# Optimization experiments

Hardware: AMD Instinct MI355X
Metric: run time of the kernel (lower is better)

## Reference

```python
import jax, jax.numpy as jnp
import numpy as np

N_NODES = 50000
N_EDGES = 800000
NFEAT = 512
NHID = 64
NHEADS = 8
NCLASS = 40
ALPHA = 0.2  # LeakyReLU slope
EPS = 1e-16  # guards isolated-node division


def setup_inputs() -> dict:
    key = jax.random.key(0)
    k = jax.random.split(key, 6)
    x = jax.random.normal(k[0], (N_NODES, NFEAT), dtype=jnp.float32)
    W_heads = jax.random.normal(k[1], (NHEADS, NFEAT, NHID), dtype=jnp.float32) * 0.05
    a_heads = jax.random.normal(k[2], (NHEADS, 2 * NHID), dtype=jnp.float32) * 0.05
    W_out = jax.random.normal(k[3], (NHEADS * NHID, NCLASS), dtype=jnp.float32) * 0.05
    a_out = jax.random.normal(k[4], (2 * NCLASS,), dtype=jnp.float32) * 0.05
    edge_index = jax.random.randint(k[5], (2, N_EDGES), 0, N_NODES, dtype=jnp.int32)
    return {"x": x, "W_heads": W_heads, "a_heads": a_heads,
            "W_out": W_out, "a_out": a_out, "edge_index": edge_index}


def _gat_layer(x, W, a, row, col, concat):
    # pyGAT sparse layer: h = xW; e_ij = exp(-LeakyReLU(a^T [h_i || h_j]));
    # out_i = sum_j e_ij h_j / sum_j e_ij   (aggregate into row, gather from col)
    D = W.shape[1]
    h = x @ W                                            # [N, D]
    score = h[row] @ a[:D] + h[col] @ a[D:]              # [E]
    e = jnp.exp(-jax.nn.leaky_relu(score, ALPHA))        # [E]
    num = jax.ops.segment_sum(e[:, None] * h[col], row, num_segments=x.shape[0])  # [N, D]
    den = jax.ops.segment_sum(e, row, num_segments=x.shape[0])                    # [N]
    out = num / (den[:, None] + EPS)
    return jax.nn.elu(out) if concat else out


def reference(x, W_heads, a_heads, W_out, a_out, edge_index):
    # dropout layers are identity in eval mode (training=False)
    row, col = edge_index[0], edge_index[1]
    heads = jax.vmap(lambda W, a: _gat_layer(x, W, a, row, col, True))(W_heads, a_heads)
    # [H, N, D] -> [N, H*D] (concat along feature dim, head-major like torch.cat)
    hcat = jnp.transpose(heads, (1, 0, 2)).reshape(x.shape[0], -1)
    return _gat_layer(hcat, W_out, a_out, row, col, False)  # [N, NCLASS]
```

## Files before the change

### kernel.cpp

```cpp
#include <hip/hip_runtime.h>
#include <hip/hip_bf16.h>

#define N_NODES 50000
#define N_EDGES 800000
#define NFEAT   512
#define NHID    64
#define NHEADS  8
#define NCLASS  40
#define HD      (NHEADS*NHID)
#define ALPHA   0.2f
#define EPS_F   1e-16f
#define NCHUNK  ((N_NODES + 255)/256)

typedef __attribute__((ext_vector_type(8))) short short8;
typedef __attribute__((ext_vector_type(4))) float floatx4;

__device__ __forceinline__ float bf2f(unsigned short u) {
    union { unsigned int i; float f; } v; v.i = ((unsigned int)u) << 16; return v.f;
}
__device__ __forceinline__ unsigned short f2bf(float f) {
    union { __hip_bfloat16 h; unsigned short u; } cv;
    cv.h = __float2bfloat16(f);
    return cv.u;
}

__device__ __forceinline__ void gload16(const unsigned short* g, short* l) {
    __builtin_amdgcn_global_load_lds(
        (const __attribute__((address_space(1))) void*)g,
        (__attribute__((address_space(3))) void*)l,
        16, 0, 0);
}

__global__ __launch_bounds__(256) void prep(const float* __restrict__ x,
                                            unsigned short* __restrict__ xb,
                                            const float* __restrict__ Wh,
                                            unsigned short* __restrict__ Wrb,
                                            const float* __restrict__ Wo,
                                            unsigned short* __restrict__ Wob,
                                            int* __restrict__ deg) {
    int idx = blockIdx.x*256 + threadIdx.x;
    if (idx < N_NODES*64) {
        const float* s = x + (size_t)idx*8;
        float4 a = *(const float4*)s, b = *(const float4*)(s+4);
        short8 h;
        h[0] = (short)f2bf(a.x); h[1] = (short)f2bf(a.y);
        h[2] = (short)f2bf(a.z); h[3] = (short)f2bf(a.w);
        h[4] = (short)f2bf(b.x); h[5] = (short)f2bf(b.y);
        h[6] = (short)f2bf(b.z); h[7] = (short)f2bf(b.w);
        *(short8*)(xb + (size_t)idx*8) = h;
    }
    if (idx < N_NODES) deg[idx] = 0;
    if (idx < 512*512) {
        int n = idx >> 9, k = idx & 511;
        int hd = n >> 6, d = n & 63;
        Wrb[idx] = f2bf(Wh[(size_t)hd*NFEAT*NHID + (size_t)k*NHID + d]);
    }
    if (idx < 64*512) {
        int n = idx >> 9, k = idx & 511;
        float v = (n < NCLASS) ? Wo[(size_t)k*NCLASS + n] : 0.f;
        Wob[idx] = f2bf(v);
    }
}

__global__ __launch_bounds__(256) void mfma_gemm1(const unsigned short* __restrict__ Abf,
                                                  const unsigned short* __restrict__ Bbf,
                                                  const float* __restrict__ a_heads,
                                                  unsigned short* __restrict__ H1,
                                                  float* __restrict__ srcdot,
                                                  float* __restrict__ dstdot, int M) {
    int id = blockIdx.x;
    int rb = (id >> 5)*8 + (id & 7);
    int cb = (id >> 3) & 3;
    int row0 = rb * 128, col0 = cb * 128;
    if (row0 >= M) return;

    __shared__ short Asl[128*32];
    __shared__ short Bsl[128*32];
    int tid  = threadIdx.x;
    int wid  = tid >> 6, lane = tid & 63;
    int lrow = lane & 15, quad = lane >> 4;
    int wm = wid & 1, wn = wid >> 1;

    int srow = wid*16 + (lane >> 2);
    int skk  = (lane & 3) * 8;
    int ar0 = row0 + srow;      ar0 = ar0 < M ? ar0 : M - 1;
    int ar1 = row0 + 64 + srow; ar1 = ar1 < M ? ar1 : M - 1;
    const unsigned short* ag0 = Abf + (size_t)ar0*512 + skk;
    const unsigned short* ag1 = Abf + (size_t)ar1*512 + skk;
    const unsigned short* bg0 = Bbf + (size_t)(col0 + srow)*512 + skk;
    const unsigned short* bg1 = Bbf + (size_t)(col0 + 64 + srow)*512 + skk;
    short* al0 = &Asl[(wid*16)*32];
    short* al1 = &Asl[(64 + wid*16)*32];
    short* bl0 = &Bsl[(wid*16)*32];
    short* bl1 = &Bsl[(64 + wid*16)*32];

    floatx4 acc[4][4];
#pragma unroll
    for (int mm = 0; mm < 4; mm++)
#pragma unroll
        for (int nn = 0; nn < 4; nn++) acc[mm][nn] = (floatx4){0.f,0.f,0.f,0.f};

    for (int k0 = 0; k0 < 512; k0 += 32) {
        gload16(ag0 + k0, al0);
        gload16(ag1 + k0, al1);
        gload16(bg0 + k0, bl0);
        gload16(bg1 + k0, bl1);
        __syncthreads();
        short8 af[4], bfr[4];
#pragma unroll
        for (int mm = 0; mm < 4; ++mm)
            af[mm] = *(const short8*)(&Asl[(wm*64 + mm*16 + lrow)*32 + quad*8]);
#pragma unroll
        for (int nn = 0; nn < 4; ++nn)
            bfr[nn] = *(const short8*)(&Bsl[(wn*64 + nn*16 + lrow)*32 + quad*8]);
#pragma unroll
        for (int mm = 0; mm < 4; ++mm)
#pragma unroll
            for (int nn = 0; nn < 4; ++nn)
                acc[mm][nn] = __builtin_amdgcn_mfma_f32_16x16x32_bf16(
                    af[mm], bfr[nn], acc[mm][nn], 0, 0, 0);
        __syncthreads();
    }

    {
        int head = (col0 >> 6) + wn;
        float a0v[4], a1v[4];
#pragma unroll
        for (int nn = 0; nn < 4; ++nn) {
            a0v[nn] = a_heads[head*128 + nn*16 + lrow];
            a1v[nn] = a_heads[head*128 + 64 + nn*16 + lrow];
        }
#pragma unroll
        for (int mm = 0; mm < 4; ++mm) {
#pragma unroll
            for (int r = 0; r < 4; ++r) {
                float s0 = 0.f, s1 = 0.f;
#pragma unroll
                for (int nn = 0; nn < 4; ++nn) {
                    float v = acc[mm][nn][r];
                    s0 = fmaf(v, a0v[nn], s0);
                    s1 = fmaf(v, a1v[nn], s1);
                }
#pragma unroll
                for (int off = 1; off < 16; off <<= 1) {
                    s0 += __shfl_xor(s0, off, 64);
                    s1 += __shfl_xor(s1, off, 64);
                }
                int grow = row0 + wm*64 + mm*16 + quad*4 + r;
                if (lrow == 0 && grow < M) {
                    srcdot[(size_t)grow*8 + head] = s0;
                    dstdot[(size_t)grow*8 + head] = s1;
                }
            }
        }
    }

#pragma unroll
    for (int mm = 0; mm < 4; ++mm) {
        int rbase = row0 + wm*64 + mm*16 + quad*4;
#pragma unroll
        for (int r = 0; r < 4; ++r) {
            int grow = rbase + r;
            if (grow < M) {
#pragma unroll
                for (int nn = 0; nn < 4; ++nn) {
                    int c = col0 + wn*64 + nn*16 + lrow;
                    H1[(size_t)grow*512 + c] = f2bf(acc[mm][nn][r]);
                }
            }
        }
    }
}

__global__ __launch_bounds__(512) void mfma_gemm2(const unsigned short* __restrict__ Abf,
                                                  const unsigned short* __restrict__ Bbf,
                                                  const float* __restrict__ a_out,
                                                  float* __restrict__ H2p,
                                                  float* __restrict__ src2,
                                                  float* __restrict__ dst2, int M) {
    __shared__ short Asl[128*32];
    __shared__ short Bsl[64*32];
    int tid  = threadIdx.x;
    int wid  = tid >> 6, lane = tid & 63;
    int lrow = lane & 15, quad = lane >> 4;
    int row0 = blockIdx.x * 128;
    if (row0 >= M) return;

    int srow = wid*16 + (lane >> 2);
    int skk  = (lane & 3) * 8;
    int ar = row0 + srow; ar = ar < M ? ar : M - 1;
    const unsigned short* ag = Abf + (size_t)ar*512 + skk;
    const unsigned short* bg = Bbf + (size_t)srow*512 + skk;
    short* al = &Asl[(wid*16)*32];
    short* bl = &Bsl[((wid & 3)*16)*32];

    floatx4 acc[4];
#pragma unroll
    for (int nn = 0; nn < 4; nn++) acc[nn] = (floatx4){0.f,0.f,0.f,0.f};

    for (int k0 = 0; k0 < 512; k0 += 32) {
        gload16(ag + k0, al);
        if (wid < 4) gload16(bg + k0, bl);
        __syncthreads();
        short8 af, bfr[4];
        af = *(const short8*)(&Asl[(wid*16 + lrow)*32 + quad*8]);
#pragma unroll
        for (int nn = 0; nn < 4; ++nn)
            bfr[nn] = *(const short8*)(&Bsl[(nn*16 + lrow)*32 + quad*8]);
#pragma unroll
        for (int nn = 0; nn < 4; ++nn)
            acc[nn] = __builtin_amdgcn_mfma_f32_16x16x32_bf16(
                af, bfr[nn], acc[nn], 0, 0, 0);
        __syncthreads();
    }

    {
        float a0v[4], a1v[4];
#pragma unroll
        for (int nn = 0; nn < 4; ++nn) {
            int c = nn*16 + lrow;
            a0v[nn] = c < NCLASS ? a_out[c] : 0.f;
            a1v[nn] = c < NCLASS ? a_out[NCLASS + c] : 0.f;
        }
#pragma unroll
        for (int r = 0; r < 4; ++r) {
            float s0 = 0.f, s1 = 0.f;
#pragma unroll
            for (int nn = 0; nn < 4; ++nn) {
                float v = acc[nn][r];
                s0 = fmaf(v, a0v[nn], s0);
                s1 = fmaf(v, a1v[nn], s1);
            }
#pragma unroll
            for (int off = 1; off < 16; off <<= 1) {
                s0 += __shfl_xor(s0, off, 64);
                s1 += __shfl_xor(s1, off, 64);
            }
            int grow = row0 + wid*16 + quad*4 + r;
            if (lrow == 0 && grow < M) {
                src2[grow] = s0;
                dst2[grow] = s1;
            }
        }
    }

#pragma unroll
    for (int nn = 0; nn < 4; ++nn) {
        int c = nn*16 + lrow;
#pragma unroll
        for (int r = 0; r < 4; ++r) {
            int grow = row0 + wid*16 + quad*4 + r;
            if (grow < M)
                H2p[(size_t)grow*64 + c] = acc[nn][r];
        }
    }
}

__global__ void histk(const int* __restrict__ row, int* __restrict__ deg) {
    int e = blockIdx.x*256 + threadIdx.x;
    if (e < N_EDGES) atomicAdd(&deg[row[e]], 1);
}
__global__ void scanA(const int* __restrict__ deg, int* __restrict__ row_ptr,
                      int* __restrict__ chunk_tot) {
    __shared__ int s[256];
    int t = threadIdx.x;
    int idx = blockIdx.x*256 + t;
    int v = (idx < N_NODES) ? deg[idx] : 0;
    s[t] = v;
    __syncthreads();
#pragma unroll
    for (int off = 1; off < 256; off <<= 1) {
        int x = (t >= off) ? s[t-off] : 0;
        __syncthreads();
        s[t] += x;
        __syncthreads();
    }
    if (idx < N_NODES) row_ptr[idx] = s[t] - v;
    if (t == 255) chunk_tot[blockIdx.x] = s[t];
}
__global__ void scanB(const int* __restrict__ chunk_tot, int* __restrict__ chunk_off,
                      int* __restrict__ row_ptr) {
    __shared__ int s[256];
    int t = threadIdx.x;
    int v = (t < NCHUNK) ? chunk_tot[t] : 0;
    s[t] = v;
    __syncthreads();
#pragma unroll
    for (int off = 1; off < 256; off <<= 1) {
        int x = (t >= off) ? s[t-off] : 0;
        __syncthreads();
        s[t] += x;
        __syncthreads();
    }
    if (t < NCHUNK) chunk_off[t] = s[t] - v;
    if (t == 255) row_ptr[N_NODES] = s[t];
}
__global__ void scanC(const int* __restrict__ chunk_off, int* __restrict__ row_ptr,
                      int* __restrict__ cursor) {
    int idx = blockIdx.x*256 + threadIdx.x;
    if (idx < N_NODES) {
        int rp = row_ptr[idx] + chunk_off[idx >> 8];
        row_ptr[idx] = rp;
        cursor[idx] = rp;
    }
}

__global__ void fillk_w1(const int* __restrict__ row, const int* __restrict__ col,
                         const float* __restrict__ srcdot, const float* __restrict__ dstdot,
                         int* __restrict__ cursor, int* __restrict__ csr_col,
                         float* __restrict__ Wcsr) {
    int e = blockIdx.x*256 + threadIdx.x;
    if (e >= N_EDGES) return;
    int r = row[e], c = col[e];
    int pos = atomicAdd(&cursor[r], 1);
    csr_col[pos] = c;
    float4 sa = *(const float4*)(srcdot + (size_t)r*8);
    float4 sb = *(const float4*)(srcdot + (size_t)r*8 + 4);
    float4 da = *(const float4*)(dstdot + (size_t)c*8);
    float4 db = *(const float4*)(dstdot + (size_t)c*8 + 4);
    float s[8] = {sa.x+da.x, sa.y+da.y, sa.z+da.z, sa.w+da.w,
                  sb.x+db.x, sb.y+db.y, sb.z+db.z, sb.w+db.w};
    float o[8];
#pragma unroll
    for (int j = 0; j < 8; j++) {
        float lr = s[j] > 0.f ? s[j] : ALPHA*s[j];
        o[j] = __expf(-lr);
    }
    *(float4*)(Wcsr + (size_t)pos*8)     = make_float4(o[0], o[1], o[2], o[3]);
    *(float4*)(Wcsr + (size_t)pos*8 + 4) = make_float4(o[4], o[5], o[6], o[7]);
}

__global__ __launch_bounds__(256) void agg1(const unsigned short* __restrict__ H1,
                                            const float* __restrict__ Wcsr,
                                            const int* __restrict__ row_ptr,
                                            const int* __restrict__ csr_col,
                                            unsigned short* __restrict__ hcatb) {
    int wave = (blockIdx.x*256 + threadIdx.x) >> 6;
    int lane = threadIdx.x & 63;
    if (wave >= N_NODES) return;
    int start = row_ptr[wave], end = row_ptr[wave+1];
    int hd = lane >> 3;
    float acc[8];
    float den = 0.f;
#pragma unroll
    for (int j = 0; j < 8; j++) acc[j] = 0.f;

    int k = start;
    for (; k + 4 <= end; k += 4) {
        int c0 = csr_col[k],   c1 = csr_col[k+1];
        int c2 = csr_col[k+2], c3 = csr_col[k+3];
        short8 hv0 = *(const short8*)(H1 + (size_t)c0*512 + lane*8);
        short8 hv1 = *(const short8*)(H1 + (size_t)c1*512 + lane*8);
        short8 hv2 = *(const short8*)(H1 + (size_t)c2*512 + lane*8);
        short8 hv3 = *(const short8*)(H1 + (size_t)c3*512 + lane*8);
        float w0 = Wcsr[(size_t)(k+0)*8 + hd];
        float w1 = Wcsr[(size_t)(k+1)*8 + hd];
        float w2 = Wcsr[(size_t)(k+2)*8 + hd];
        float w3 = Wcsr[(size_t)(k+3)*8 + hd];
        den += (w0 + w1) + (w2 + w3);
#pragma unroll
        for (int j = 0; j < 8; j++) {
            acc[j] = fmaf(w0, bf2f((unsigned short)hv0[j]), acc[j]);
            acc[j] = fmaf(w1, bf2f((unsigned short)hv1[j]), acc[j]);
            acc[j] = fmaf(w2, bf2f((unsigned short)hv2[j]), acc[j]);
            acc[j] = fmaf(w3, bf2f((unsigned short)hv3[j]), acc[j]);
        }
    }
    for (; k < end; ++k) {
        int c = csr_col[k];
        short8 hv = *(const short8*)(H1 + (size_t)c*512 + lane*8);
        float w = Wcsr[(size_t)k*8 + hd];
        den += w;
#pragma unroll
        for (int j = 0; j < 8; j++)
            acc[j] = fmaf(w, bf2f((unsigned short)hv[j]), acc[j]);
    }
    float rden = 1.f / (den + EPS_F);
    short8 o8;
#pragma unroll
    for (int j = 0; j < 8; j++) {
        float o = acc[j] * rden;
        o = o > 0.f ? o : (__expf(o) - 1.f);
        o8[j] = (short)f2bf(o);
    }
    *(short8*)(hcatb + (size_t)wave*HD + lane*8) = o8;
}

__global__ __launch_bounds__(256) void agg2(const float* __restrict__ H2p,
                                            const float* __restrict__ src2,
                                            const float* __restrict__ dst2,
                                            const int* __restrict__ row_ptr,
                                            const int* __restrict__ csr_col,
                                            float* __restrict__ out) {
    int wave = (blockIdx.x*256 + threadIdx.x) >> 6;
    int lane = threadIdx.x & 63;
    if (wave >= N_NODES) return;
    int start = row_ptr[wave], end = row_ptr[wave+1];
    int deg = end - start;
    float s2i = src2[wave];
    int l = lane < NCLASS ? lane : 0;
    float acc = 0.f, den = 0.f;

    int colreg = 0;
    if (deg > 0) colreg = csr_col[start + (lane < deg ? lane : deg - 1)];

#define AG2_G1(T, H, IDX) do { \
    int cg_ = __builtin_amdgcn_readlane(colreg, (IDX)); \
    T = dst2[cg_]; \
    H = H2p[(size_t)cg_*64 + l]; \
} while(0)
#define AG2_C1(T, H) do { \
    float t_ = s2i + (T); \
    t_ = t_ > 0.f ? t_ : ALPHA*t_; \
    float w_ = __expf(-t_); \
    den += w_; acc = fmaf(w_, (H), acc); \
} while(0)
#define AG2_G8(T0,T1,T2,T3,T4,T5,T6,T7,H0,H1,H2,H3,H4,H5,H6,H7,BASE) do { \
    AG2_G1(T0,H0,(BASE));   AG2_G1(T1,H1,(BASE)+1); \
    AG2_G1(T2,H2,(BASE)+2); AG2_G1(T3,H3,(BASE)+3); \
    AG2_G1(T4,H4,(BASE)+4); AG2_G1(T5,H5,(BASE)+5); \
    AG2_G1(T6,H6,(BASE)+6); AG2_G1(T7,H7,(BASE)+7); \
} while(0)
#define AG2_C8(T0,T1,T2,T3,T4,T5,T6,T7,H0,H1,H2,H3,H4,H5,H6,H7) do { \
    AG2_C1(T0,H0); AG2_C1(T1,H1); AG2_C1(T2,H2); AG2_C1(T3,H3); \
    AG2_C1(T4,H4); AG2_C1(T5,H5); AG2_C1(T6,H6); AG2_C1(T7,H7); \
} while(0)

    int lim = deg < 64 ? deg : 64;
    int nb = lim >> 3;
    int k = start;
    float ta0,ta1,ta2,ta3,ta4,ta5,ta6,ta7, ga0,ga1,ga2,ga3,ga4,ga5,ga6,ga7;
    float tb0,tb1,tb2,tb3,tb4,tb5,tb6,tb7, gb0,gb1,gb2,gb3,gb4,gb5,gb6,gb7;
    if (nb > 0) {
        AG2_G8(ta0,ta1,ta2,ta3,ta4,ta5,ta6,ta7, ga0,ga1,ga2,ga3,ga4,ga5,ga6,ga7, 0);
        int b = 1;
        for (; b + 1 < nb; b += 2) {
            AG2_G8(tb0,tb1,tb2,tb3,tb4,tb5,tb6,tb7, gb0,gb1,gb2,gb3,gb4,gb5,gb6,gb7, b*8);
            AG2_C8(ta0,ta1,ta2,ta3,ta4,ta5,ta6,ta7, ga0,ga1,ga2,ga3,ga4,ga5,ga6,ga7);
            AG2_G8(ta0,ta1,ta2,ta3,ta4,ta5,ta6,ta7, ga0,ga1,ga2,ga3,ga4,ga5,ga6,ga7, (b+1)*8);
            AG2_C8(tb0,tb1,tb2,tb3,tb4,tb5,tb6,tb7, gb0,gb1,gb2,gb3,gb4,gb5,gb6,gb7);
        }
        if (b < nb) {
            AG2_G8(tb0,tb1,tb2,tb3,tb4,tb5,tb6,tb7, gb0,gb1,gb2,gb3,gb4,gb5,gb6,gb7, b*8);
            AG2_C8(ta0,ta1,ta2,ta3,ta4,ta5,ta6,ta7, ga0,ga1,ga2,ga3,ga4,ga5,ga6,ga7);
            AG2_C8(tb0,tb1,tb2,tb3,tb4,tb5,tb6,tb7, gb0,gb1,gb2,gb3,gb4,gb5,gb6,gb7);
        } else {
            AG2_C8(ta0,ta1,ta2,ta3,ta4,ta5,ta6,ta7, ga0,ga1,ga2,ga3,ga4,ga5,ga6,ga7);
        }
        k = start + nb*8;
    }
    for (; k < end; ++k) {
        int c_ = (k - start < 64) ? __builtin_amdgcn_readlane(colreg, k - start)
                                  : csr_col[k];
        float t = dst2[c_];
        float h = H2p[(size_t)c_*64 + l];
        AG2_C1(t, h);
    }
#undef AG2_G1
#undef AG2_C1
#undef AG2_G8
#undef AG2_C8

    if (lane < NCLASS)
        out[(size_t)wave*NCLASS + lane] = acc / (den + EPS_F);
}

extern "C" void kernel_launch(void* const* d_in, const int* in_sizes, int n_in,
                              void* d_out, int out_size, void* d_ws, size_t ws_size,
                              hipStream_t stream) {
    const float* x       = (const float*)d_in[0];
    const float* W_heads = (const float*)d_in[1];
    const float* a_heads = (const float*)d_in[2];
    const float* W_out   = (const float*)d_in[3];
    const float* a_out   = (const float*)d_in[4];
    const int*   ei      = (const int*)d_in[5];
    const int*   row     = ei;
    const int*   col     = ei + N_EDGES;
    float* out = (float*)d_out;

    char* ws = (char*)d_ws;
    size_t off = 0;
    auto alloc = [&](size_t bytes) {
        char* p = ws + off;
        off = (off + bytes + 255) & ~(size_t)255;
        return p;
    };
    unsigned short* Wrb   = (unsigned short*)alloc((size_t)512*512*2);
    unsigned short* Wob   = (unsigned short*)alloc((size_t)64*512*2);
    unsigned short* H1    = (unsigned short*)alloc((size_t)N_NODES*HD*2);
    unsigned short* xb    = (unsigned short*)alloc((size_t)N_NODES*NFEAT*2);
    unsigned short* hcatb = xb;
    float* srcdot  = (float*)alloc((size_t)N_NODES*NHEADS*4);
    float* dstdot  = (float*)alloc((size_t)N_NODES*NHEADS*4);
    float* Wcsr    = (float*)alloc((size_t)N_EDGES*NHEADS*4);
    int*   deg     = (int*)alloc((size_t)N_NODES*4);
    int*   row_ptr = (int*)alloc((size_t)(N_NODES+1)*4);
    int*   cursor  = (int*)alloc((size_t)N_NODES*4);
    int*   ctot    = (int*)alloc(256*4);
    int*   coff    = (int*)alloc(256*4);
    int*   csr_col = (int*)alloc((size_t)N_EDGES*4);
    float* H2p     = (float*)alloc((size_t)N_NODES*64*4);
    float* src2    = (float*)alloc((size_t)N_NODES*4);
    float* dst2    = (float*)alloc((size_t)N_NODES*4);
    (void)ws_size;

    const int EB = (N_EDGES + 255)/256;
    const int WB = (N_NODES*64 + 255)/256;

    prep<<<(N_NODES*64 + 255)/256, 256, 0, stream>>>(x, xb, W_heads, Wrb,
                                                     W_out, Wob, deg);
    {
        int rtiles = (N_NODES + 127)/128;
        int nblk = ((rtiles + 7)/8) * 32;
        mfma_gemm1<<<nblk, 256, 0, stream>>>(xb, Wrb, a_heads, H1,
                                             srcdot, dstdot, N_NODES);
    }

    histk<<<EB, 256, 0, stream>>>(row, deg);
    scanA<<<NCHUNK, 256, 0, stream>>>(deg, row_ptr, ctot);
    scanB<<<1, 256, 0, stream>>>(ctot, coff, row_ptr);
    scanC<<<NCHUNK, 256, 0, stream>>>(coff, row_ptr, cursor);
    fillk_w1<<<EB, 256, 0, stream>>>(row, col, srcdot, dstdot, cursor,
                                     csr_col, Wcsr);

    agg1<<<WB, 256, 0, stream>>>(H1, Wcsr, row_ptr, csr_col, hcatb);

    mfma_gemm2<<<(N_NODES + 127)/128, 512, 0, stream>>>(hcatb, Wob, a_out,
                                                        H2p, src2, dst2, N_NODES);
    agg2<<<WB, 256, 0, stream>>>(H2p, src2, dst2, row_ptr, csr_col, out);
}
```

Baseline: 486.6 us.

## Use XOR-swizzled 64-wide K tiles in GEMMs and store H2 as bf16

Both MFMA GEMMs now stage 64-element K slices per iteration into LDS with an XOR swizzle of the 16-byte groups, which halves the number of barrier pairs and is meant to avoid LDS bank conflicts on fragment reads. The second-layer projection H2 is now written as bf16 instead of fp32, halving the bytes agg2 gathers per edge. In exchange it doubles LDS use per block, which may lower occupancy, and it adds bf16 rounding to the layer-2 features.

Result: faster. 474.2 us (-2.5%).

```diff
diff --git a/kernel.cpp b/kernel.cpp
--- a/kernel.cpp
+++ b/kernel.cpp
@@ -74,25 +74,29 @@
     int row0 = rb * 128, col0 = cb * 128;
     if (row0 >= M) return;
 
-    __shared__ short Asl[128*32];
-    __shared__ short Bsl[128*32];
+    __shared__ short Asl[128*64];
+    __shared__ short Bsl[128*64];
     int tid  = threadIdx.x;
     int wid  = tid >> 6, lane = tid & 63;
     int lrow = lane & 15, quad = lane >> 4;
     int wm = wid & 1, wn = wid >> 1;
 
-    int srow = wid*16 + (lane >> 2);
-    int skk  = (lane & 3) * 8;
-    int ar0 = row0 + srow;      ar0 = ar0 < M ? ar0 : M - 1;
-    int ar1 = row0 + 64 + srow; ar1 = ar1 < M ? ar1 : M - 1;
-    const unsigned short* ag0 = Abf + (size_t)ar0*512 + skk;
-    const unsigned short* ag1 = Abf + (size_t)ar1*512 + skk;
-    const unsigned short* bg0 = Bbf + (size_t)(col0 + srow)*512 + skk;
-    const unsigned short* bg1 = Bbf + (size_t)(col0 + 64 + srow)*512 + skk;
-    short* al0 = &Asl[(wid*16)*32];
-    short* al1 = &Asl[(64 + wid*16)*32];
-    short* bl0 = &Bsl[(wid*16)*32];
-    short* bl1 = &Bsl[(64 + wid*16)*32];
+    int lr = lane >> 3, g = lane & 7;
+    int gg8 = ((g ^ lr) << 3);
+    const unsigned short* agp[4];
+    const unsigned short* bgp[4];
+    short* alp[4];
+    short* blp[4];
+#pragma unroll
+    for (int i = 0; i < 4; ++i) {
+        int cq = wid*4 + i;
+        int r  = cq*8 + lr;
+        int arow = row0 + r; arow = arow < M ? arow : M - 1;
+        agp[i] = Abf + (size_t)arow*512 + gg8;
+        bgp[i] = Bbf + (size_t)(col0 + r)*512 + gg8;
+        alp[i] = &Asl[(cq*8)*64];
+        blp[i] = &Bsl[(cq*8)*64];
+    }
 
     floatx4 acc[4][4];
 #pragma unroll
@@ -100,25 +104,30 @@
 #pragma unroll
         for (int nn = 0; nn < 4; nn++) acc[mm][nn] = (floatx4){0.f,0.f,0.f,0.f};
 
-    for (int k0 = 0; k0 < 512; k0 += 32) {
-        gload16(ag0 + k0, al0);
-        gload16(ag1 + k0, al1);
-        gload16(bg0 + k0, bl0);
-        gload16(bg1 + k0, bl1);
-        __syncthreads();
-        short8 af[4], bfr[4];
-#pragma unroll
-        for (int mm = 0; mm < 4; ++mm)
-            af[mm] = *(const short8*)(&Asl[(wm*64 + mm*16 + lrow)*32 + quad*8]);
-#pragma unroll
-        for (int nn = 0; nn < 4; ++nn)
-            bfr[nn] = *(const short8*)(&Bsl[(wn*64 + nn*16 + lrow)*32 + quad*8]);
-#pragma unroll
-        for (int mm = 0; mm < 4; ++mm)
+    for (int k0 = 0; k0 < 512; k0 += 64) {
+#pragma unroll
+        for (int i = 0; i < 4; ++i) {
+            gload16(agp[i] + k0, alp[i]);
+            gload16(bgp[i] + k0, blp[i]);
+        }
+        __syncthreads();
+#pragma unroll
+        for (int ks = 0; ks < 2; ++ks) {
+            int gsw = ((ks*4 + quad) ^ (lrow & 7)) * 8;
+            short8 af[4], bfr[4];
+#pragma unroll
+            for (int mm = 0; mm < 4; ++mm)
+                af[mm] = *(const short8*)(&Asl[(wm*64 + mm*16 + lrow)*64 + gsw]);
 #pragma unroll
             for (int nn = 0; nn < 4; ++nn)
-                acc[mm][nn] = __builtin_amdgcn_mfma_f32_16x16x32_bf16(
-                    af[mm], bfr[nn], acc[mm][nn], 0, 0, 0);
+                bfr[nn] = *(const short8*)(&Bsl[(wn*64 + nn*16 + lrow)*64 + gsw]);
+#pragma unroll
+            for (int mm = 0; mm < 4; ++mm)
+#pragma unroll
+                for (int nn = 0; nn < 4; ++nn)
+                    acc[mm][nn] = __builtin_amdgcn_mfma_f32_16x16x32_bf16(
+                        af[mm], bfr[nn], acc[mm][nn], 0, 0, 0);
+        }
         __syncthreads();
     }
 
@@ -175,42 +184,50 @@
 __global__ __launch_bounds__(512) void mfma_gemm2(const unsigned short* __restrict__ Abf,
                                                   const unsigned short* __restrict__ Bbf,
                                                   const float* __restrict__ a_out,
-                                                  float* __restrict__ H2p,
+                                                  unsigned short* __restrict__ H2b,
                                                   float* __restrict__ src2,
                                                   float* __restrict__ dst2, int M) {
-    __shared__ short Asl[128*32];
-    __shared__ short Bsl[64*32];
+    __shared__ short Asl[128*64];
+    __shared__ short Bsl[64*64];
     int tid  = threadIdx.x;
     int wid  = tid >> 6, lane = tid & 63;
     int lrow = lane & 15, quad = lane >> 4;
     int row0 = blockIdx.x * 128;
     if (row0 >= M) return;
 
-    int srow = wid*16 + (lane >> 2);
-    int skk  = (lane & 3) * 8;
-    int ar = row0 + srow; ar = ar < M ? ar : M - 1;
-    const unsigned short* ag = Abf + (size_t)ar*512 + skk;
-    const unsigned short* bg = Bbf + (size_t)srow*512 + skk;
-    short* al = &Asl[(wid*16)*32];
-    short* bl = &Bsl[((wid & 3)*16)*32];
+    int lr = lane >> 3, g = lane & 7;
+    int gg8 = ((g ^ lr) << 3);
+    int ar0 = row0 + wid*16 + lr;     ar0 = ar0 < M ? ar0 : M - 1;
+    int ar1 = row0 + wid*16 + 8 + lr; ar1 = ar1 < M ? ar1 : M - 1;
+    const unsigned short* agp0 = Abf + (size_t)ar0*512 + gg8;
+    const unsigned short* agp1 = Abf + (size_t)ar1*512 + gg8;
+    const unsigned short* bgp  = Bbf + (size_t)(wid*8 + lr)*512 + gg8;
+    short* al0 = &Asl[(wid*16)*64];
+    short* al1 = &Asl[(wid*16 + 8)*64];
+    short* bl  = &Bsl[(wid*8)*64];
 
     floatx4 acc[4];
 #pragma unroll
     for (int nn = 0; nn < 4; nn++) acc[nn] = (floatx4){0.f,0.f,0.f,0.f};
 
-    for (int k0 = 0; k0 < 512; k0 += 32) {
-        gload16(ag + k0, al);
-        if (wid < 4) gload16(bg + k0, bl);
-        __syncthreads();
-        short8 af, bfr[4];
-        af = *(const short8*)(&Asl[(wid*16 + lrow)*32 + quad*8]);
-#pragma unroll
-        for (int nn = 0; nn < 4; ++nn)
-            bfr[nn] = *(const short8*)(&Bsl[(nn*16 + lrow)*32 + quad*8]);
-#pragma unroll
-        for (int nn = 0; nn < 4; ++nn)
-            acc[nn] = __builtin_amdgcn_mfma_f32_16x16x32_bf16(
-                af, bfr[nn], acc[nn], 0, 0, 0);
+    for (int k0 = 0; k0 < 512; k0 += 64) {
+        gload16(agp0 + k0, al0);
+        gload16(agp1 + k0, al1);
+        gload16(bgp + k0, bl);
+        __syncthreads();
+#pragma unroll
+        for (int ks = 0; ks < 2; ++ks) {
+            int gsw = ((ks*4 + quad) ^ (lrow & 7)) * 8;
+            short8 af, bfr[4];
+            af = *(const short8*)(&Asl[(wid*16 + lrow)*64 + gsw]);
+#pragma unroll
+            for (int nn = 0; nn < 4; ++nn)
+                bfr[nn] = *(const short8*)(&Bsl[(nn*16 + lrow)*64 + gsw]);
+#pragma unroll
+            for (int nn = 0; nn < 4; ++nn)
+                acc[nn] = __builtin_amdgcn_mfma_f32_16x16x32_bf16(
+                    af, bfr[nn], acc[nn], 0, 0, 0);
+        }
         __syncthreads();
     }
 
@@ -251,7 +268,7 @@
         for (int r = 0; r < 4; ++r) {
             int grow = row0 + wid*16 + quad*4 + r;
             if (grow < M)
-                H2p[(size_t)grow*64 + c] = acc[nn][r];
+                H2b[(size_t)grow*64 + c] = f2bf(acc[nn][r]);
         }
     }
 }
@@ -386,7 +403,7 @@
     *(short8*)(hcatb + (size_t)wave*HD + lane*8) = o8;
 }
 
-__global__ __launch_bounds__(256) void agg2(const float* __restrict__ H2p,
+__global__ __launch_bounds__(256) void agg2(const unsigned short* __restrict__ H2b,
                                             const float* __restrict__ src2,
                                             const float* __restrict__ dst2,
                                             const int* __restrict__ row_ptr,
@@ -407,7 +424,7 @@
 #define AG2_G1(T, H, IDX) do { \
     int cg_ = __builtin_amdgcn_readlane(colreg, (IDX)); \
     T = dst2[cg_]; \
-    H = H2p[(size_t)cg_*64 + l]; \
+    H = bf2f(H2b[(size_t)cg_*64 + l]); \
 } while(0)
 #define AG2_C1(T, H) do { \
     float t_ = s2i + (T); \
@@ -453,7 +470,7 @@
         int c_ = (k - start < 64) ? __builtin_amdgcn_readlane(colreg, k - start)
                                   : csr_col[k];
         float t = dst2[c_];
-        float h = H2p[(size_t)c_*64 + l];
+        float h = bf2f(H2b[(size_t)c_*64 + l]);
         AG2_C1(t, h);
     }
 #undef AG2_G1
@@ -499,7 +516,7 @@
     int*   ctot    = (int*)alloc(256*4);
     int*   coff    = (int*)alloc(256*4);
     int*   csr_col = (int*)alloc((size_t)N_EDGES*4);
-    float* H2p     = (float*)alloc((size_t)N_NODES*64*4);
+    unsigned short* H2b = (unsigned short*)alloc((size_t)N_NODES*64*2);
     float* src2    = (float*)alloc((size_t)N_NODES*4);
     float* dst2    = (float*)alloc((size_t)N_NODES*4);
     (void)ws_size;
@@ -526,6 +543,6 @@
     agg1<<<WB, 256, 0, stream>>>(H1, Wcsr, row_ptr, csr_col, hcatb);
 
     mfma_gemm2<<<(N_NODES + 127)/128, 512, 0, stream>>>(hcatb, Wob, a_out,
-                                                        H2p, src2, dst2, N_NODES);
-    agg2<<<WB, 256, 0, stream>>>(H2p, src2, dst2, row_ptr, csr_col, out);
-}
+                                                        H2b, src2, dst2, N_NODES);
+    agg2<<<WB, 256, 0, stream>>>(H2b, src2, dst2, row_ptr, csr_col, out);
+}
```
